# Kernel tuning notes

Measured on AMD Instinct MI355X. Metric: run time of the kernel, lower is better.

The kernel has to match this reference:

```python
import jax, jax.numpy as jnp
import numpy as np

SCALE = 1.0  # args.scale


def setup_inputs() -> dict:
    key = jax.random.key(0)
    k1, k2, k3, k4, k5 = jax.random.split(key, 5)
    B, S, D, R, LR = 4, 2048, 2048, 2048, 16  # batch, seq, column(emb), row(out), lora rank
    inp = jax.random.normal(k1, (B, S, D), dtype=jnp.float32)
    weight = jax.random.normal(k2, (R, D), dtype=jnp.float32) * (1.0 / np.sqrt(D))
    bias = jax.random.normal(k3, (R,), dtype=jnp.float32)
    lora_right = jax.random.normal(k4, (B, D, LR), dtype=jnp.float32) * 0.02
    lora_left = jax.random.normal(k5, (B, LR, R), dtype=jnp.float32) * 0.02
    return {"input": inp, "weight": weight, "bias": bias,
            "lora_right": lora_right, "lora_left": lora_left}


def reference(input, weight, bias, lora_right, lora_left):
    # Base linear: x @ W^T + b  -> [B, S, R]
    x = jnp.einsum('bsd,rd->bsr', input, weight) + bias
    # Per-sample low-rank LoRA chain: (input @ right) @ left, batched
    t = jnp.einsum('bsd,bdk->bsk', input, lora_right)   # [B, S, LR]
    y = jnp.einsum('bsk,bkr->bsr', t, lora_left)        # [B, S, R]
    # L2-normalize each token vector along the last dim, then scale
    y = y / jnp.linalg.norm(y, axis=-1, keepdims=True)
    y = y * SCALE
    return x + y
```

## Files before the change

kernel.cpp:

```cpp
#include <hip/hip_runtime.h>
#include <hip/hip_bf16.h>

#define SCALE_V 1.0f

typedef __bf16 bf16v8 __attribute__((ext_vector_type(8)));
typedef float f32v4 __attribute__((ext_vector_type(4)));

typedef const __attribute__((address_space(1))) void* gas_t;
typedef __attribute__((address_space(3))) void* las_t;
#define ASYNC_COPY16(g, l) \
    __builtin_amdgcn_global_load_lds((gas_t)(g), (las_t)(l), 16, 0, 0)
#define FENCE() asm volatile("" ::: "memory")
#define MFMA __builtin_amdgcn_mfma_f32_16x16x32_bf16

__global__ __launch_bounds__(256) void transpose_lr_kernel(
    const float* __restrict__ lright, __bf16* __restrict__ lrT) {
    __shared__ float tile[16][273];
    const int b = blockIdx.y;
    const int d0 = blockIdx.x * 256;
    const int t = threadIdx.x;
    const float* src = lright + (size_t)b * 32768 + (size_t)d0 * 16;
    #pragma unroll
    for (int j = 0; j < 16; ++j) {
        tile[t & 15][j * 16 + (t >> 4)] = src[j * 256 + t];
    }
    __syncthreads();
    const int k = t >> 4, dcol = t & 15;
    __bf16* dst = lrT + (size_t)b * 32768 + (size_t)k * 2048 + d0;
    #pragma unroll
    for (int j = 0; j < 16; ++j) {
        dst[dcol + j * 16] = (__bf16)tile[k][dcol + j * 16];
    }
}

__global__ __launch_bounds__(256, 4) void prep_kernel(
    const float* __restrict__ inp, const float* __restrict__ wgt,
    const __bf16* __restrict__ lrT, const float* __restrict__ lleft,
    __bf16* __restrict__ abf, __bf16* __restrict__ wbf,
    float* __restrict__ tout, float* __restrict__ gpart) {
    __shared__ float sm[256];
    const int bid = blockIdx.x;
    const int tid = threadIdx.x;

    if (bid < 2048) {
        const int row0 = bid * 4;
        const int b = row0 >> 11;
        const __bf16* lt = lrT + (size_t)b * 32768;

        float x[4][8];
        #pragma unroll
        for (int rr = 0; rr < 4; ++rr) {
            const float* p = inp + (size_t)(row0 + rr) * 2048 + tid * 8;
            float4 a0 = *(const float4*)p;
            float4 a1 = *(const float4*)(p + 4);
            x[rr][0] = a0.x; x[rr][1] = a0.y; x[rr][2] = a0.z; x[rr][3] = a0.w;
            x[rr][4] = a1.x; x[rr][5] = a1.y; x[rr][6] = a1.z; x[rr][7] = a1.w;
            bf16v8 v;
            #pragma unroll
            for (int i = 0; i < 8; ++i) v[i] = (__bf16)x[rr][i];
            *(bf16v8*)(abf + (size_t)(row0 + rr) * 2048 + tid * 8) = v;
        }

        float v[64];
        #pragma unroll
        for (int k = 0; k < 16; ++k) {
            bf16v8 lb = *(const bf16v8*)(lt + (size_t)k * 2048 + tid * 8);
            float lv[8];
            #pragma unroll
            for (int i = 0; i < 8; ++i) lv[i] = (float)lb[i];
            #pragma unroll
            for (int rr = 0; rr < 4; ++rr) {
                float s = 0.f;
                #pragma unroll
                for (int i = 0; i < 8; ++i) s += x[rr][i] * lv[i];
                v[rr * 16 + k] = s;
            }
        }

        const int lane = tid & 63;
        const int w = tid >> 6;
        #pragma unroll
        for (int s = 1, cnt = 64; s < 64; s <<= 1, cnt >>= 1) {
            const int half = cnt >> 1;
            const bool up = (lane & s) != 0;
            #pragma unroll
            for (int i = 0; i < 32; ++i) {
                if (i < half) {
                    float keep = up ? v[i + half] : v[i];
                    float give = up ? v[i] : v[i + half];
                    v[i] = keep + __shfl_xor(give, s, 64);
                }
            }
        }
        const int rev = ((lane & 1) << 5) | ((lane & 2) << 3) | ((lane & 4) << 1) |
                        ((lane & 8) >> 1) | ((lane & 16) >> 3) | ((lane & 32) >> 5);
        sm[w * 64 + rev] = v[0];
        __syncthreads();
        if (tid < 64) {
            tout[(size_t)row0 * 16 + tid] =
                sm[tid] + sm[64 + tid] + sm[128 + tid] + sm[192 + tid];
        }
    } else if (bid < 4096) {
        const int i = ((bid - 2048) * 256 + tid) * 8;
        float4 x0 = *(const float4*)(wgt + i);
        float4 x1 = *(const float4*)(wgt + i + 4);
        bf16v8 v;
        v[0] = (__bf16)x0.x; v[1] = (__bf16)x0.y; v[2] = (__bf16)x0.z; v[3] = (__bf16)x0.w;
        v[4] = (__bf16)x1.x; v[5] = (__bf16)x1.y; v[6] = (__bf16)x1.z; v[7] = (__bf16)x1.w;
        *(bf16v8*)(wbf + i) = v;
    } else {
        const int g = bid - 4096;
        const int b = g >> 3, c = g & 7;
        const int k = tid >> 4, j = tid & 15;
        const float* pk = lleft + ((size_t)b * 16 + k) * 2048 + c * 256;
        const float* pj = lleft + ((size_t)b * 16 + j) * 2048 + c * 256;
        float s = 0.f;
        #pragma unroll 4
        for (int r = 0; r < 256; r += 4) {
            float4 a = *(const float4*)(pk + r);
            float4 d = *(const float4*)(pj + r);
            s += a.x * d.x + a.y * d.y + a.z * d.z + a.w * d.w;
        }
        gpart[((size_t)b * 8 + c) * 256 + tid] = s;
    }
}

__global__ __launch_bounds__(512, 2) void gemm_ep_kernel(
    const __bf16* __restrict__ abf, const __bf16* __restrict__ wbf,
    const float* __restrict__ bias, const float* __restrict__ traw,
    const float* __restrict__ gpart, const float* __restrict__ lleft,
    float* __restrict__ out) {
    __shared__ __attribute__((aligned(16))) char smem[131072];

    const int tid  = threadIdx.x;
    const int w    = tid >> 6;
    const int lane = tid & 63;
    const int l3   = lane >> 3, l7 = lane & 7;
    const int wm   = w >> 2;
    const int wn   = w & 3;
    const int fr   = lane & 15;

    const int xcd   = blockIdx.x & 7;
    const int local = blockIdx.x >> 3;
    const int tile_n = local & 7;
    const int tile_m = (xcd << 2) | (local >> 3);
    const int row0 = tile_m * 256;
    const int col0 = tile_n * 256;

    const int cswz = ((l7 ^ l3) * 8);
    const size_t aG0 = (size_t)(row0 + 8 * w + l3) * 2048 + cswz;
    const int bCh = 64 * (w >> 2) + 8 * (w & 3);
    const size_t bG0 = (size_t)(col0 + bCh + l3) * 2048 + cswz;
    char* const aDst = smem + 8 * w * 128 + lane * 16;
    char* const bDst = smem + 65536 + bCh * 128 + lane * 16;

#define STAGE_A(BUFOFF, S, KKEL)                                                         \
    do {                                                                                 \
        ASYNC_COPY16(abf + aG0 + (size_t)((S)*64) * 2048 + (KKEL),  aDst + (BUFOFF) + (S)*8192);          \
        ASYNC_COPY16(abf + aG0 + (size_t)((S)*64 + 128) * 2048 + (KKEL), aDst + (BUFOFF) + (S)*8192 + 16384); \
    } while (0)
#define STAGE_B(BUFOFF, S, KKEL)                                                         \
    do {                                                                                 \
        ASYNC_COPY16(wbf + bG0 + (size_t)((S)*32) * 2048 + (KKEL),  bDst + (BUFOFF) + (S)*4096);          \
        ASYNC_COPY16(wbf + bG0 + (size_t)((S)*32 + 128) * 2048 + (KKEL), bDst + (BUFOFF) + (S)*4096 + 16384); \
    } while (0)

    const int kx0 = (((lane >> 4) * 16) ^ (l7 << 4));
    const int kx1 = ((64 + (lane >> 4) * 16) ^ (l7 << 4));
    const char* const aRd = smem + (wm * 128 + fr) * 128;
    const char* const bRd = smem + 65536 + (wn * 64 + fr) * 128;

    f32v4 acc[8][4];
    #pragma unroll
    for (int m = 0; m < 8; ++m)
        #pragma unroll
        for (int n = 0; n < 4; ++n) {
            acc[m][n][0] = 0.f; acc[m][n][1] = 0.f;
            acc[m][n][2] = 0.f; acc[m][n][3] = 0.f;
        }

    STAGE_A(0, 0, 0);
    STAGE_B(0, 0, 0);
    STAGE_B(0, 1, 0);
    STAGE_A(0, 1, 0);
    STAGE_B(32768, 0, 64);
    STAGE_B(32768, 1, 64);
    STAGE_A(32768, 0, 64);
    asm volatile("s_waitcnt vmcnt(6)" ::: "memory");
    FENCE(); __builtin_amdgcn_s_barrier(); FENCE();

    #pragma unroll 2
    for (int kt = 0; kt < 32; ++kt) {
        const int bo = (kt & 1) * 32768;
        const int bn = bo ^ 32768;
        const size_t kk1 = (size_t)((kt + 1) & 31) * 64;
        const size_t kk2 = (size_t)((kt + 2) & 31) * 64;
        bf16v8 afA[4][2], afB[4][2], bl[2][2], bh[2][2];

        #pragma unroll
        for (int m = 0; m < 4; ++m) {
            afA[m][0] = *(const bf16v8*)(aRd + bo + m * 2048 + kx0);
            afA[m][1] = *(const bf16v8*)(aRd + bo + m * 2048 + kx1);
        }
        #pragma unroll
        for (int n = 0; n < 2; ++n) {
            bl[n][0] = *(const bf16v8*)(bRd + bo + n * 2048 + kx0);
            bl[n][1] = *(const bf16v8*)(bRd + bo + n * 2048 + kx1);
            bh[n][0] = *(const bf16v8*)(bRd + bo + (n + 2) * 2048 + kx0);
            bh[n][1] = *(const bf16v8*)(bRd + bo + (n + 2) * 2048 + kx1);
        }
        STAGE_A(bn, 1, kk1);
        __builtin_amdgcn_s_setprio(1);
        #pragma unroll
        for (int m = 0; m < 4; ++m)
            #pragma unroll
            for (int n = 0; n < 2; ++n) {
                acc[m][n] = MFMA(afA[m][0], bl[n][0], acc[m][n], 0, 0, 0);
                acc[m][n] = MFMA(afA[m][1], bl[n][1], acc[m][n], 0, 0, 0);
            }
        __builtin_amdgcn_s_setprio(0);
        FENCE(); __builtin_amdgcn_s_barrier(); FENCE();

        __builtin_amdgcn_s_setprio(1);
        #pragma unroll
        for (int m = 0; m < 4; ++m)
            #pragma unroll
            for (int n = 0; n < 2; ++n) {
                acc[m][n + 2] = MFMA(afA[m][0], bh[n][0], acc[m][n + 2], 0, 0, 0);
                acc[m][n + 2] = MFMA(afA[m][1], bh[n][1], acc[m][n + 2], 0, 0, 0);
            }
        __builtin_amdgcn_s_setprio(0);
        #pragma unroll
        for (int m = 0; m < 4; ++m) {
            afB[m][0] = *(const bf16v8*)(aRd + bo + (m + 4) * 2048 + kx0);
            afB[m][1] = *(const bf16v8*)(aRd + bo + (m + 4) * 2048 + kx1);
        }
        STAGE_B(bo, 0, kk2);
        FENCE(); __builtin_amdgcn_s_barrier(); FENCE();

        __builtin_amdgcn_s_setprio(1);
        #pragma unroll
        for (int m = 0; m < 4; ++m)
            #pragma unroll
            for (int n = 0; n < 2; ++n) {
                acc[m + 4][n + 2] = MFMA(afB[m][0], bh[n][0], acc[m + 4][n + 2], 0, 0, 0);
                acc[m + 4][n + 2] = MFMA(afB[m][1], bh[n][1], acc[m + 4][n + 2], 0, 0, 0);
            }
        __builtin_amdgcn_s_setprio(0);
        STAGE_B(bo, 1, kk2);
        FENCE(); __builtin_amdgcn_s_barrier(); FENCE();

        __builtin_amdgcn_s_setprio(1);
        #pragma unroll
        for (int m = 0; m < 4; ++m)
            #pragma unroll
            for (int n = 0; n < 2; ++n) {
                acc[m + 4][n] = MFMA(afB[m][0], bl[n][0], acc[m + 4][n], 0, 0, 0);
                acc[m + 4][n] = MFMA(afB[m][1], bl[n][1], acc[m + 4][n], 0, 0, 0);
            }
        __builtin_amdgcn_s_setprio(0);
        STAGE_A(bo, 0, kk2);
        asm volatile("s_waitcnt vmcnt(6)" ::: "memory");
        FENCE(); __builtin_amdgcn_s_barrier(); FENCE();
    }

    asm volatile("s_waitcnt vmcnt(0)" ::: "memory");
    __syncthreads();
    {
        bf16v8 zv;
        #pragma unroll
        for (int i = 0; i < 8; ++i) zv[i] = (__bf16)0.f;

        __bf16* tE  = (__bf16*)smem;
        __bf16* LE  = (__bf16*)(smem + 20480);
        float*  gsf = (float*)(smem + 40960);
        const int bb = row0 >> 11;

        if (tid < 256) {
            float g = 0.f;
            #pragma unroll
            for (int c = 0; c < 8; ++c) g += gpart[((size_t)bb * 8 + c) * 256 + tid];
            gsf[tid] = g;
        }
        {
            const int r = tid >> 1;
            const int h = (tid & 1) * 8;
            const float* lp = lleft + ((size_t)bb * 16 + h) * 2048 + col0 + r;
            bf16v8 lv;
            #pragma unroll
            for (int i = 0; i < 8; ++i) lv[i] = (__bf16)lp[(size_t)i * 2048];
            *(bf16v8*)(LE + r * 40 + h) = lv;
            *(bf16v8*)(LE + r * 40 + 16 + h) = zv;
        }
        __syncthreads();
        if (tid < 256) {
            const float* tp = traw + (size_t)(row0 + tid) * 16;
            float4 a0 = *(const float4*)(tp);
            float4 a1 = *(const float4*)(tp + 4);
            float4 a2 = *(const float4*)(tp + 8);
            float4 a3 = *(const float4*)(tp + 12);
            float tv[16] = {a0.x, a0.y, a0.z, a0.w, a1.x, a1.y, a1.z, a1.w,
                            a2.x, a2.y, a2.z, a2.w, a3.x, a3.y, a3.z, a3.w};
            float q = 0.f;
            #pragma unroll
            for (int k = 0; k < 16; ++k) {
                float s = 0.f;
                #pragma unroll
                for (int j = 0; j < 16; ++j) s += gsf[k * 16 + j] * tv[j];
                q += tv[k] * s;
            }
            const float sc = SCALE_V * rsqrtf(q);
            bf16v8 t0v, t1v;
            #pragma unroll
            for (int i = 0; i < 8; ++i) {
                t0v[i] = (__bf16)(tv[i] * sc);
                t1v[i] = (__bf16)(tv[8 + i] * sc);
            }
            *(bf16v8*)(tE + tid * 40)      = t0v;
            *(bf16v8*)(tE + tid * 40 + 8)  = t1v;
            *(bf16v8*)(tE + tid * 40 + 16) = zv;
            *(bf16v8*)(tE + tid * 40 + 24) = zv;
        }
        __syncthreads();
    }
    {
        const __bf16* tE = (const __bf16*)smem;
        const __bf16* LE = (const __bf16*)(smem + 20480);
        const int ko = (lane >> 4) * 8;
        bf16v8 bE[4];
        #pragma unroll
        for (int n = 0; n < 4; ++n)
            bE[n] = *(const bf16v8*)(LE + (wn * 64 + n * 16 + fr) * 40 + ko);
        #pragma unroll
        for (int m = 0; m < 8; ++m) {
            bf16v8 aE = *(const bf16v8*)(tE + (wm * 128 + m * 16 + fr) * 40 + ko);
            #pragma unroll
            for (int n = 0; n < 4; ++n)
                acc[m][n] = MFMA(aE, bE[n], acc[m][n], 0, 0, 0);
        }
    }

    #pragma unroll
    for (int n = 0; n < 4; ++n) {
        const int gc = col0 + wn * 64 + n * 16 + fr;
        const float bv = bias[gc];
        #pragma unroll
        for (int m = 0; m < 8; ++m) {
            #pragma unroll
            for (int j = 0; j < 4; ++j) {
                const int gr = row0 + wm * 128 + m * 16 + (lane >> 4) * 4 + j;
                out[(size_t)gr * 2048 + gc] = acc[m][n][j] + bv;
            }
        }
    }
#undef STAGE_A
#undef STAGE_B
}

extern "C" void kernel_launch(void* const* d_in, const int* in_sizes, int n_in,
                              void* d_out, int out_size, void* d_ws, size_t ws_size,
                              hipStream_t stream) {
    const float* inp  = (const float*)d_in[0];
    const float* wgt  = (const float*)d_in[1];
    const float* bias = (const float*)d_in[2];
    const float* lrt  = (const float*)d_in[3];
    const float* llf  = (const float*)d_in[4];
    float* out = (float*)d_out;

    char* ws = (char*)d_ws;
    __bf16* abf  = (__bf16*)ws;
    __bf16* wbf  = (__bf16*)(ws + 33554432);
    float*  tbuf = (float*)(ws + 41943040);
    float*  gprt = (float*)(ws + 42467328);
    __bf16* lrT  = (__bf16*)(ws + 42500096);

    transpose_lr_kernel<<<dim3(8, 4), 256, 0, stream>>>(lrt, lrT);
    prep_kernel<<<4128, 256, 0, stream>>>(inp, wgt, lrT, llf, abf, wbf, tbuf, gprt);
    gemm_ep_kernel<<<dim3(256), 512, 0, stream>>>(abf, wbf, bias, tbuf, gprt, llf, out);
}
```

Measured before the change: 103.6 us.

## Stagger MFMA and memory phases between wave groups in GEMM main loop

Splits waves by their wm index into two groups that run each phase in opposite order. One group issues MFMAs first and then its LDS reads and async global-to-LDS copies, while the other does memory first and then MFMAs. The aim is ping-pong scheduling, where one wave group keeps the matrix cores busy while the other uses the memory pipes, reducing contention inside each barrier interval. This duplicates code, which increases instruction footprint, and it can change register pressure or add branch divergence overhead.

```diff
diff --git a/kernel.cpp b/kernel.cpp
--- a/kernel.cpp
+++ b/kernel.cpp
@@ -206,60 +206,125 @@
         for (int n = 0; n < 2; ++n) {
             bl[n][0] = *(const bf16v8*)(bRd + bo + n * 2048 + kx0);
             bl[n][1] = *(const bf16v8*)(bRd + bo + n * 2048 + kx1);
-            bh[n][0] = *(const bf16v8*)(bRd + bo + (n + 2) * 2048 + kx0);
-            bh[n][1] = *(const bf16v8*)(bRd + bo + (n + 2) * 2048 + kx1);
-        }
-        STAGE_A(bn, 1, kk1);
-        __builtin_amdgcn_s_setprio(1);
-        #pragma unroll
-        for (int m = 0; m < 4; ++m)
+        }
+        if (wm == 0) {
+            STAGE_A(bn, 1, kk1);
+            __builtin_amdgcn_s_setprio(1);
+            #pragma unroll
+            for (int m = 0; m < 4; ++m)
+                #pragma unroll
+                for (int n = 0; n < 2; ++n) {
+                    acc[m][n] = MFMA(afA[m][0], bl[n][0], acc[m][n], 0, 0, 0);
+                    acc[m][n] = MFMA(afA[m][1], bl[n][1], acc[m][n], 0, 0, 0);
+                }
+            __builtin_amdgcn_s_setprio(0);
             #pragma unroll
             for (int n = 0; n < 2; ++n) {
-                acc[m][n] = MFMA(afA[m][0], bl[n][0], acc[m][n], 0, 0, 0);
-                acc[m][n] = MFMA(afA[m][1], bl[n][1], acc[m][n], 0, 0, 0);
-            }
-        __builtin_amdgcn_s_setprio(0);
+                bh[n][0] = *(const bf16v8*)(bRd + bo + (n + 2) * 2048 + kx0);
+                bh[n][1] = *(const bf16v8*)(bRd + bo + (n + 2) * 2048 + kx1);
+            }
+        } else {
+            #pragma unroll
+            for (int n = 0; n < 2; ++n) {
+                bh[n][0] = *(const bf16v8*)(bRd + bo + (n + 2) * 2048 + kx0);
+                bh[n][1] = *(const bf16v8*)(bRd + bo + (n + 2) * 2048 + kx1);
+            }
+            STAGE_A(bn, 1, kk1);
+            __builtin_amdgcn_s_setprio(1);
+            #pragma unroll
+            for (int m = 0; m < 4; ++m)
+                #pragma unroll
+                for (int n = 0; n < 2; ++n) {
+                    acc[m][n] = MFMA(afA[m][0], bl[n][0], acc[m][n], 0, 0, 0);
+                    acc[m][n] = MFMA(afA[m][1], bl[n][1], acc[m][n], 0, 0, 0);
+                }
+            __builtin_amdgcn_s_setprio(0);
+        }
         FENCE(); __builtin_amdgcn_s_barrier(); FENCE();
 
-        __builtin_amdgcn_s_setprio(1);
-        #pragma unroll
-        for (int m = 0; m < 4; ++m)
-            #pragma unroll
-            for (int n = 0; n < 2; ++n) {
-                acc[m][n + 2] = MFMA(afA[m][0], bh[n][0], acc[m][n + 2], 0, 0, 0);
-                acc[m][n + 2] = MFMA(afA[m][1], bh[n][1], acc[m][n + 2], 0, 0, 0);
-            }
-        __builtin_amdgcn_s_setprio(0);
-        #pragma unroll
-        for (int m = 0; m < 4; ++m) {
-            afB[m][0] = *(const bf16v8*)(aRd + bo + (m + 4) * 2048 + kx0);
-            afB[m][1] = *(const bf16v8*)(aRd + bo + (m + 4) * 2048 + kx1);
-        }
-        STAGE_B(bo, 0, kk2);
+        if (wm == 0) {
+            __builtin_amdgcn_s_setprio(1);
+            #pragma unroll
+            for (int m = 0; m < 4; ++m)
+                #pragma unroll
+                for (int n = 0; n < 2; ++n) {
+                    acc[m][n + 2] = MFMA(afA[m][0], bh[n][0], acc[m][n + 2], 0, 0, 0);
+                    acc[m][n + 2] = MFMA(afA[m][1], bh[n][1], acc[m][n + 2], 0, 0, 0);
+                }
+            __builtin_amdgcn_s_setprio(0);
+            #pragma unroll
+            for (int m = 0; m < 4; ++m) {
+                afB[m][0] = *(const bf16v8*)(aRd + bo + (m + 4) * 2048 + kx0);
+                afB[m][1] = *(const bf16v8*)(aRd + bo + (m + 4) * 2048 + kx1);
+            }
+            STAGE_B(bo, 0, kk2);
+        } else {
+            #pragma unroll
+            for (int m = 0; m < 4; ++m) {
+                afB[m][0] = *(const bf16v8*)(aRd + bo + (m + 4) * 2048 + kx0);
+                afB[m][1] = *(const bf16v8*)(aRd + bo + (m + 4) * 2048 + kx1);
+            }
+            STAGE_B(bo, 0, kk2);
+            __builtin_amdgcn_s_setprio(1);
+            #pragma unroll
+            for (int m = 0; m < 4; ++m)
+                #pragma unroll
+                for (int n = 0; n < 2; ++n) {
+                    acc[m][n + 2] = MFMA(afA[m][0], bh[n][0], acc[m][n + 2], 0, 0, 0);
+                    acc[m][n + 2] = MFMA(afA[m][1], bh[n][1], acc[m][n + 2], 0, 0, 0);
+                }
+            __builtin_amdgcn_s_setprio(0);
+        }
         FENCE(); __builtin_amdgcn_s_barrier(); FENCE();
 
-        __builtin_amdgcn_s_setprio(1);
-        #pragma unroll
-        for (int m = 0; m < 4; ++m)
-            #pragma unroll
-            for (int n = 0; n < 2; ++n) {
-                acc[m + 4][n + 2] = MFMA(afB[m][0], bh[n][0], acc[m + 4][n + 2], 0, 0, 0);
-                acc[m + 4][n + 2] = MFMA(afB[m][1], bh[n][1], acc[m + 4][n + 2], 0, 0, 0);
-            }
-        __builtin_amdgcn_s_setprio(0);
-        STAGE_B(bo, 1, kk2);
+        if (wm == 0) {
+            __builtin_amdgcn_s_setprio(1);
+            #pragma unroll
+            for (int m = 0; m < 4; ++m)
+                #pragma unroll
+                for (int n = 0; n < 2; ++n) {
+                    acc[m + 4][n + 2] = MFMA(afB[m][0], bh[n][0], acc[m + 4][n + 2], 0, 0, 0);
+                    acc[m + 4][n + 2] = MFMA(afB[m][1], bh[n][1], acc[m + 4][n + 2], 0, 0, 0);
+                }
+            __builtin_amdgcn_s_setprio(0);
+            STAGE_B(bo, 1, kk2);
+        } else {
+            STAGE_B(bo, 1, kk2);
+            __builtin_amdgcn_s_setprio(1);
+            #pragma unroll
+            for (int m = 0; m < 4; ++m)
+                #pragma unroll
+                for (int n = 0; n < 2; ++n) {
+                    acc[m + 4][n + 2] = MFMA(afB[m][0], bh[n][0], acc[m + 4][n + 2], 0, 0, 0);
+                    acc[m + 4][n + 2] = MFMA(afB[m][1], bh[n][1], acc[m + 4][n + 2], 0, 0, 0);
+                }
+            __builtin_amdgcn_s_setprio(0);
+        }
         FENCE(); __builtin_amdgcn_s_barrier(); FENCE();
 
-        __builtin_amdgcn_s_setprio(1);
-        #pragma unroll
-        for (int m = 0; m < 4; ++m)
-            #pragma unroll
-            for (int n = 0; n < 2; ++n) {
-                acc[m + 4][n] = MFMA(afB[m][0], bl[n][0], acc[m + 4][n], 0, 0, 0);
-                acc[m + 4][n] = MFMA(afB[m][1], bl[n][1], acc[m + 4][n], 0, 0, 0);
-            }
-        __builtin_amdgcn_s_setprio(0);
-        STAGE_A(bo, 0, kk2);
+        if (wm == 0) {
+            __builtin_amdgcn_s_setprio(1);
+            #pragma unroll
+            for (int m = 0; m < 4; ++m)
+                #pragma unroll
+                for (int n = 0; n < 2; ++n) {
+                    acc[m + 4][n] = MFMA(afB[m][0], bl[n][0], acc[m + 4][n], 0, 0, 0);
+                    acc[m + 4][n] = MFMA(afB[m][1], bl[n][1], acc[m + 4][n], 0, 0, 0);
+                }
+            __builtin_amdgcn_s_setprio(0);
+            STAGE_A(bo, 0, kk2);
+        } else {
+            STAGE_A(bo, 0, kk2);
+            __builtin_amdgcn_s_setprio(1);
+            #pragma unroll
+            for (int m = 0; m < 4; ++m)
+                #pragma unroll
+                for (int n = 0; n < 2; ++n) {
+                    acc[m + 4][n] = MFMA(afB[m][0], bl[n][0], acc[m + 4][n], 0, 0, 0);
+                    acc[m + 4][n] = MFMA(afB[m][1], bl[n][1], acc[m + 4][n], 0, 0, 0);
+                }
+            __builtin_amdgcn_s_setprio(0);
+        }
         asm volatile("s_waitcnt vmcnt(6)" ::: "memory");
         FENCE(); __builtin_amdgcn_s_barrier(); FENCE();
     }
```

After: 194.7 us. +87.9%, slower.
